# Kernel optimization log

Hardware: AMD Instinct MI355X
Metric: run time of the kernel (lower is better)

## Reference

```python
import jax, jax.numpy as jnp
import numpy as np

ROPE_DIM = 64
ROPE_THETA = 10000.0
SLIDING_WINDOW = 1024
_K_MASK = jnp.finfo(jnp.bfloat16).min


def _pos_embeddings(positions, head_dim, rope_theta):
    # positions: [B, T] -> sin, cos: [B, T, head_dim]
    fraction = jnp.arange(0, head_dim, 2, dtype=jnp.float32) / head_dim
    inv_freq = 1.0 / (rope_theta ** fraction)
    sinusoid = jnp.einsum('BT,k->BTk', positions.astype(jnp.float32), inv_freq,
                          precision=jax.lax.Precision.HIGHEST)
    sin = jnp.sin(sinusoid); cos = jnp.cos(sinusoid)
    return jnp.concatenate([sin, sin], -1), jnp.concatenate([cos, cos], -1)


def _rotate_half(x):
    x1, x2 = x[..., :x.shape[-1] // 2], x[..., x.shape[-1] // 2:]
    return jnp.concatenate([-x2, x1], -1)


def _apply_rope_partial(x, sin, cos, rope_dim):
    x_rope, x_nope = x[..., :rope_dim], x[..., rope_dim:]
    sin = sin[:, :, None, :]; cos = cos[:, :, None, :]
    x_rope = x_rope * cos + _rotate_half(x_rope) * sin
    return jnp.concatenate([x_rope, x_nope], -1).astype(x.dtype)


def setup_inputs() -> dict:
    key = jax.random.key(0)
    ks = jax.random.split(key, 6)
    B, T, D = 2, 2048, 2048
    N, K, H, Hv = 16, 4, 128, 128
    S = 2048  # cache size
    sc = 0.02
    return {
        'x': jax.random.normal(ks[0], (B, T, D), jnp.float32),
        'wq': jax.random.normal(ks[1], (D, N, H), jnp.float32) * sc,
        'wk': jax.random.normal(ks[2], (D, K, H), jnp.float32) * sc,
        'wv': jax.random.normal(ks[3], (D, K, Hv), jnp.float32) * sc,
        'wo': jax.random.normal(ks[4], (N, Hv, D), jnp.float32) * sc,
        'sink_bias': jnp.zeros((N,), jnp.float32),
        'k_cache': jnp.zeros((B, S, K, H), jnp.float32),
        'v_cache': jnp.zeros((B, S, K, Hv), jnp.float32),
        'segment_ids': jnp.ones((B, T), jnp.int32),
        'cur_ind': 0,
        'start_ind': -jnp.ones((B,), jnp.int32),
    }


def reference(x, wq, wk, wv, wo, sink_bias, k_cache, v_cache,
              segment_ids, cur_ind, start_ind):
    B, T, D = x.shape
    N, H = wq.shape[1], wq.shape[2]
    K, Hv = wk.shape[1], wv.shape[2]
    n_rep = N // K
    scaling = H ** -0.5
    cur_ind = jnp.asarray(cur_ind, jnp.int32)

    q = jnp.einsum('BTD,DNH->BTNH', x, wq)
    k = jnp.einsum('BSD,DKH->BSKH', x, wk)
    v = jnp.einsum('BSD,DKV->BSKV', x, wv)

    # left pads / positions from segment ids
    left_pads = jnp.sum(jnp.cumsum(segment_ids != 0, axis=-1) == 0, -1).astype(jnp.int32)
    start = jnp.where(start_ind < 0, left_pads, start_ind)
    pos = jax.vmap(lambda row: jnp.where(row != 0,
                                         jnp.arange(T, dtype=jnp.int32) - jnp.argmax(row).astype(jnp.int32),
                                         2 ** 30))(segment_ids) + cur_ind
    sin, cos = _pos_embeddings(pos, ROPE_DIM, ROPE_THETA)
    q = _apply_rope_partial(q, sin, cos, ROPE_DIM)
    k = _apply_rope_partial(k, sin, cos, ROPE_DIM)

    # KV cache append
    kc = jax.lax.dynamic_update_slice(k_cache, k, (0, cur_ind, 0, 0))
    vc = jax.lax.dynamic_update_slice(v_cache, v, (0, cur_ind, 0, 0))
    S = kc.shape[1]

    # GQA repeat
    kr = jnp.repeat(kc[:, :, :, None, :], n_rep, axis=3).reshape(B, S, N, H)
    vr = jnp.repeat(vc[:, :, :, None, :], n_rep, axis=3).reshape(B, S, N, Hv)

    logits = jnp.einsum('BTNH,BSNH->BTNS', q, kr) * scaling

    q_pos = cur_ind + jnp.arange(T, dtype=jnp.int32)[None, :] - start[:, None]
    ts = jnp.arange(S, dtype=jnp.int32)
    kv_seg = (ts[None, :] >= start[:, None]) & (ts[None, :] < cur_ind + T)
    k_pos = ts[None, :] - start[:, None]
    causal = k_pos[:, None, :] <= q_pos[:, :, None]
    seg_mask = kv_seg[:, None, :] == segment_ids[:, :, None]
    window = k_pos[:, None, :] >= q_pos[:, :, None] - (SLIDING_WINDOW - 1)
    final_mask = causal & seg_mask & window  # [B, T, S]
    logits = jnp.where(final_mask[:, :, None, :], logits, _K_MASK)

    # attention sink bias: extra softmax slot per head
    sink = jnp.broadcast_to(sink_bias[None, None, :, None], (B, T, N, 1))
    logits = jnp.concatenate([logits, sink], axis=-1)
    weights = jax.nn.softmax(logits.astype(jnp.float32), axis=-1).astype(logits.dtype)
    weights = weights[..., :-1]

    attn = jnp.einsum('BTNS,BSNV->BTNV', weights, vr)
    return jnp.einsum('BTNV,NVD->BTD', attn, wo)
```

## Files before the change

### kernel.cpp

```cpp
#include <hip/hip_runtime.h>
#include <hip/hip_bf16.h>
#include <stdint.h>

#define BB 2
#define TT 2048
#define DD 2048
#define NHQ 16
#define KH 4
#define HD 128
#define SS 2048
#define WINDOW 1024
#define M2FIX 12.0f
#define QSC_LOG2E 0.12751751f
#define LOG2E 1.4426950408889634f
#define NLOG2F 0.4152410118609203f

typedef __attribute__((ext_vector_type(8))) short bf16x8;
typedef __attribute__((ext_vector_type(4))) float f32x4;
typedef __attribute__((ext_vector_type(16))) float f32x16;

#define MFMA16(a, b, c) __builtin_amdgcn_mfma_f32_16x16x32_bf16(a, b, c, 0, 0, 0)
#define MFMA32(a, b, c) __builtin_amdgcn_mfma_f32_32x32x16_bf16(a, b, c, 0, 0, 0)

__device__ __forceinline__ ushort f2bf(float f) {
  uint32_t u = __float_as_uint(f);
  u += 0x7FFF + ((u >> 16) & 1);
  return (ushort)(u >> 16);
}
__device__ __forceinline__ ushort f2bf_trunc(float f) {
  return (ushort)(__float_as_uint(f) >> 16);
}
__device__ __forceinline__ float bf2f(ushort h) {
  return __uint_as_float(((uint32_t)h) << 16);
}

__device__ __forceinline__ void async_copy16(const ushort* g, ushort* l) {
  __builtin_amdgcn_global_load_lds(
      (const __attribute__((address_space(1))) uint32_t*)g,
      (__attribute__((address_space(3))) uint32_t*)l, 16, 0, 0);
}

__device__ __forceinline__ void tr_tile(const float* __restrict__ in,
                                        ushort* __restrict__ out,
                                        int C, int ldo, int cx, int cy) {
  __shared__ float tile[32][36];
  int t = threadIdx.x;
  int r0 = cy * 32, c0 = cx * 32;
  int row = t >> 3, c4 = (t & 7) * 4;
  float4 v = *(const float4*)&in[(size_t)(r0 + row) * C + c0 + c4];
  *(float4*)&tile[row][c4] = v;
  __syncthreads();
  int oc = t >> 3, or4 = (t & 7) * 4;
  ushort4 o;
  o.x = f2bf(tile[or4 + 0][oc]);
  o.y = f2bf(tile[or4 + 1][oc]);
  o.z = f2bf(tile[or4 + 2][oc]);
  o.w = f2bf(tile[or4 + 3][oc]);
  *(ushort4*)&out[(size_t)(c0 + oc) * ldo + r0 + or4] = o;
}

__global__ void prep_fused(const float* __restrict__ x, const float* __restrict__ wq,
                           const float* __restrict__ wk, const float* __restrict__ wv,
                           const float* __restrict__ wo, const int* __restrict__ seg,
                           const int* __restrict__ start_ind, ushort* __restrict__ xb,
                           ushort* __restrict__ WcatT, ushort* __restrict__ WoT,
                           int* __restrict__ meta) {
  int bz = blockIdx.x;
  int tid = threadIdx.x;
  if (bz < 2) {
    __shared__ int red[256];
    int b = bz;
    int first = TT;
    for (int t = tid; t < TT; t += 256)
      if (seg[b * TT + t] != 0) first = min(first, t);
    red[tid] = first;
    __syncthreads();
    for (int s = 128; s > 0; s >>= 1) {
      if (tid < s) red[tid] = min(red[tid], red[tid + s]);
      __syncthreads();
    }
    if (tid == 0) {
      int fi = red[0];
      int st = start_ind[b] < 0 ? fi : start_ind[b];
      meta[b * 2 + 0] = st;
      meta[b * 2 + 1] = (fi >= TT) ? 0 : fi;
    }
    return;
  }
  bz -= 2;
  if (bz < 2048) {
#pragma unroll
    for (int p = 0; p < 4; p++) {
      int i = bz * 1024 + p * 256 + tid;
      float4 v = ((const float4*)x)[i];
      ushort4 o;
      o.x = f2bf(v.x); o.y = f2bf(v.y); o.z = f2bf(v.z); o.w = f2bf(v.w);
      ((ushort4*)xb)[i] = o;
    }
    return;
  }
  bz -= 2048;
  if (bz < 4096) { tr_tile(wq, WcatT, 2048, 2048, bz & 63, bz >> 6); return; }
  bz -= 4096;
  if (bz < 1024) { tr_tile(wk, WcatT + (size_t)2048 * 2048, 512, 2048, bz & 15, bz >> 4); return; }
  bz -= 1024;
  if (bz < 1024) { tr_tile(wv, WcatT + (size_t)2560 * 2048, 512, 2048, bz & 15, bz >> 4); return; }
  bz -= 1024;
  tr_tile(wo, WoT, 2048, 2048, bz & 63, bz >> 6);
}

__global__ __launch_bounds__(256) void gemm_qkv(const ushort* __restrict__ A,
                                                const ushort* __restrict__ Bt,
                                                const int* __restrict__ seg,
                                                const int* __restrict__ cur_p,
                                                const int* __restrict__ meta,
                                                ushort* __restrict__ qa,
                                                ushort* __restrict__ ka,
                                                ushort* __restrict__ vat) {
  const int K = DD;
  __shared__ ushort SH[16640];
  ushort* As = SH;
  ushort* Bs = SH + 8192;
  float* posf_s = (float*)(SH + 16384);
  int tid = threadIdx.x;
  int lane = tid & 63, wave = tid >> 6;
  int wr = wave >> 1, wc = wave & 1;
  int orig = blockIdx.y * 24 + blockIdx.x;
  int wid = (orig & 7) * 96 + (orig >> 3);
  int by = wid / 24, bx = wid - by * 24;
  int row0 = by * 128, col0 = bx * 128;
  int l31 = lane & 31, khalf = lane >> 5, lx8 = l31 & 7;
  int cur = cur_p[0];

  if (tid < 128) {
    int m = row0 + tid;
    int bb = m >> 11, t = m & 2047;
    int segv = seg[m];
    int first = meta[bb * 2 + 1];
    posf_s[tid] = (segv != 0) ? (float)(t - first + cur) : 1073741824.0f;
  }

  f32x16 acc[2][2];
#pragma unroll
  for (int i = 0; i < 2; i++)
#pragma unroll
    for (int j = 0; j < 2; j++)
#pragma unroll
      for (int e = 0; e < 16; e++) acc[i][j][e] = 0.f;

  int srow = tid >> 3, scol = tid & 7;
  int ssw = (scol ^ (srow & 7)) * 8;
  const ushort* Ag = A  + (size_t)(row0 + srow) * K + ssw;
  const ushort* Bg = Bt + (size_t)(col0 + srow) * K + ssw;
  ushort* AsD = As + tid * 8;
  ushort* BsD = Bs + tid * 8;

  for (int kc = 0; kc < K; kc += 64) {
    __syncthreads();
#pragma unroll
    for (int p = 0; p < 4; p++)
      async_copy16(Ag + kc + (size_t)(p * 32) * K, AsD + p * 2048);
#pragma unroll
    for (int p = 0; p < 4; p++)
      async_copy16(Bg + kc + (size_t)(p * 32) * K, BsD + p * 2048);
    __syncthreads();
#pragma unroll
    for (int ks = 0; ks < 4; ks++) {
      bf16x8 af[2], bfm[2];
      int ch = (ks * 2 + khalf) ^ lx8;
#pragma unroll
      for (int i = 0; i < 2; i++)
        af[i] = *(const bf16x8*)(As + (wr * 64 + i * 32 + l31) * 64 + ch * 8);
#pragma unroll
      for (int j = 0; j < 2; j++)
        bfm[j] = *(const bf16x8*)(Bs + (wc * 64 + j * 32 + l31) * 64 + ch * 8);
#pragma unroll
      for (int i = 0; i < 2; i++)
#pragma unroll
        for (int j = 0; j < 2; j++)
          acc[i][j] = MFMA32(af[i], bfm[j], acc[i][j]);
    }
  }

  int cb0 = col0 + wc * 64;
  int region = (cb0 < 2048) ? 0 : (cb0 < 2560 ? 1 : 2);

  if (region <= 1) {
    bool ropehalf = ((cb0 & 64) == 0);
    int hbase = cb0 & 64;
    float invf = exp2f(-NLOG2F * (float)l31);
#pragma unroll
    for (int i = 0; i < 2; i++) {
#pragma unroll
      for (int reg = 0; reg < 16; reg++) {
        int rloc = wr * 64 + i * 32 + (reg & 3) + 8 * (reg >> 2) + 4 * khalf;
        int m = row0 + rloc;
        int b = m >> 11, t = m & 2047;
        float v0 = acc[i][0][reg], v1 = acc[i][1][reg];
        if (ropehalf) {
          float posf = posf_s[rloc];
          float sn, cs;
          __sincosf(posf * invf, &sn, &cs);
          float n0 = v0 * cs - v1 * sn;
          v1 = v1 * cs + v0 * sn;
          v0 = n0;
        }
        if (region == 0) {
          int head = cb0 >> 7;
          size_t base = ((size_t)(b * NHQ + head) * TT + t) * HD + hbase;
          qa[base + l31]      = f2bf(v0 * QSC_LOG2E);
          qa[base + 32 + l31] = f2bf(v1 * QSC_LOG2E);
        } else {
          int head = (cb0 - 2048) >> 7;
          size_t rowbase = ((size_t)(b * KH + head) * SS + t) * HD;
          int sw = t & 7;
          int c0x = hbase + l31, c1x = hbase + 32 + l31;
          ka[rowbase + ((((c0x >> 3) ^ sw) << 3) | (c0x & 7))] = f2bf(v0);
          ka[rowbase + ((((c1x >> 3) ^ sw) << 3) | (c1x & 7))] = f2bf(v1);
        }
      }
    }
  } else {
    __syncthreads();
    ushort* TB = SH;
    int hbase = wc * 64;
#pragma unroll
    for (int i = 0; i < 2; i++)
#pragma unroll
      for (int reg = 0; reg < 16; reg++) {
        int rloc = wr * 64 + i * 32 + (reg & 3) + 8 * (reg >> 2) + 4 * khalf;
        int h0 = hbase + l31, h1 = hbase + 32 + l31;
        TB[h0 * 128 + (rloc ^ ((h0 & 15) << 3))] = f2bf(acc[i][0][reg]);
        TB[h1 * 128 + (rloc ^ ((h1 & 15) << 3))] = f2bf(acc[i][1][reg]);
      }
    __syncthreads();
    int headv = (col0 - 2560) >> 7;
    int bv = row0 >> 11;
    ushort* vout = vat + (size_t)(bv * KH + headv) * HD * SS + (row0 & 2047);
#pragma unroll
    for (int pass = 0; pass < 8; pass++) {
      int idx = pass * 256 + tid;
      int h = idx >> 4, cc = idx & 15;
      int s64 = cc >> 3, c = cc & 7;
      bf16x8 vd = *(const bf16x8*)(TB + h * 128 + (s64 ^ ((h >> 3) & 1)) * 64 + c * 8);
      *(bf16x8*)(vout + (size_t)h * SS + s64 * 64 + c * 8) = vd;
    }
  }
}

template <int OUT_F32>
__global__ __launch_bounds__(256) void gemm_bt(const ushort* __restrict__ A,
                                               const ushort* __restrict__ Bt,
                                               void* __restrict__ Cout,
                                               int M, int N, int K) {
  __shared__ ushort As[128 * 64];
  __shared__ ushort Bs[128 * 64];
  int tid = threadIdx.x;
  int lane = tid & 63, wave = tid >> 6;
  int wr = wave >> 1, wc = wave & 1;
  int orig = blockIdx.y * gridDim.x + blockIdx.x;
  int nwg = gridDim.x * gridDim.y;
  int cpx = nwg >> 3;
  int wid = (orig & 7) * cpx + (orig >> 3);
  int by = wid / gridDim.x, bx = wid - by * gridDim.x;
  int row0 = by * 128, col0 = bx * 128;
  int l31 = lane & 31, khalf = lane >> 5, lx8 = l31 & 7;

  f32x16 acc[2][2];
#pragma unroll
  for (int i = 0; i < 2; i++)
#pragma unroll
    for (int j = 0; j < 2; j++)
#pragma unroll
      for (int e = 0; e < 16; e++) acc[i][j][e] = 0.f;

  int srow = tid >> 3, scol = tid & 7;
  int ssw = (scol ^ (srow & 7)) * 8;
  const ushort* Ag = A  + (size_t)(row0 + srow) * K + ssw;
  const ushort* Bg = Bt + (size_t)(col0 + srow) * K + ssw;
  ushort* AsD = As + tid * 8;
  ushort* BsD = Bs + tid * 8;

  for (int kc = 0; kc < K; kc += 64) {
    __syncthreads();
#pragma unroll
    for (int p = 0; p < 4; p++)
      async_copy16(Ag + kc + (size_t)(p * 32) * K, AsD + p * 2048);
#pragma unroll
    for (int p = 0; p < 4; p++)
      async_copy16(Bg + kc + (size_t)(p * 32) * K, BsD + p * 2048);
    __syncthreads();
#pragma unroll
    for (int ks = 0; ks < 4; ks++) {
      bf16x8 af[2], bfm[2];
      int ch = (ks * 2 + khalf) ^ lx8;
#pragma unroll
      for (int i = 0; i < 2; i++)
        af[i] = *(const bf16x8*)(As + (wr * 64 + i * 32 + l31) * 64 + ch * 8);
#pragma unroll
      for (int j = 0; j < 2; j++)
        bfm[j] = *(const bf16x8*)(Bs + (wc * 64 + j * 32 + l31) * 64 + ch * 8);
#pragma unroll
      for (int i = 0; i < 2; i++)
#pragma unroll
        for (int j = 0; j < 2; j++)
          acc[i][j] = MFMA32(af[i], bfm[j], acc[i][j]);
    }
  }

#pragma unroll
  for (int i = 0; i < 2; i++)
#pragma unroll
    for (int reg = 0; reg < 16; reg++) {
      int r = row0 + wr * 64 + i * 32 + (reg & 3) + 8 * (reg >> 2) + 4 * khalf;
#pragma unroll
      for (int j = 0; j < 2; j++) {
        int c = col0 + wc * 64 + j * 32 + l31;
        float v = acc[i][j][reg];
        if (OUT_F32)
          ((float*)Cout)[(size_t)r * N + c] = v;
        else
          ((ushort*)Cout)[(size_t)r * N + c] = f2bf(v);
      }
    }
}

__global__ __launch_bounds__(256) void flash_attn(
    const ushort* __restrict__ qa, const ushort* __restrict__ ka,
    const ushort* __restrict__ vat, const float* __restrict__ sink_bias,
    const int* __restrict__ seg, const int* __restrict__ cur_p,
    const int* __restrict__ meta, ushort* __restrict__ Obuf) {
  __shared__ ushort Ks[64 * 128];
  __shared__ ushort VT[128 * 64];
  __shared__ ushort Ps[4 * 16 * 64];

  int bx = blockIdx.x;
  int xcd = bx & 7;
  int b = xcd >> 2, kb = xcd & 3;
  int idx = bx >> 3;
  int g = idx & 31, s = idx >> 5;
  int n = kb * 4 + (g & 3);
  int j = g >> 2;
  int qt = (s == 0) ? j : (s == 1) ? (15 - j) : (s == 2) ? (16 + j) : (31 - j);
  int t0 = qt * 64;
  int cur = cur_p[0];
  int start = meta[b * 2];

  int tid = threadIdx.x, lane = tid & 63, w = tid >> 6;
  int lcol = lane & 15, quad = lane >> 4, lx = lcol & 7;
  int t0w = t0 + w * 16;

  const ushort* qbase = qa + (size_t)(b * NHQ + n) * TT * HD;
  const ushort* kbase = ka + (size_t)(b * KH + kb) * SS * HD;
  const ushort* vtb   = vat + (size_t)(b * KH + kb) * HD * SS;

  bf16x8 qf[4];
  {
    const ushort* qrow = qbase + (size_t)(t0w + lcol) * HD + quad * 8;
#pragma unroll
    for (int c = 0; c < 4; c++) qf[c] = *(const bf16x8*)(qrow + c * 32);
  }

  int segq[4], trow[4];
#pragma unroll
  for (int r = 0; r < 4; r++) {
    trow[r] = t0w + quad * 4 + r;
    segq[r] = seg[b * TT + trow[r]];
  }
  int seg1 = __all(segq[0] == 1 && segq[1] == 1 && segq[2] == 1 && segq[3] == 1);

  f32x4 oacc[8], lacc;
#pragma unroll
  for (int ob = 0; ob < 8; ob++) { f32x4 z = {0.f, 0.f, 0.f, 0.f}; oacc[ob] = z; }
  { f32x4 z = {0.f, 0.f, 0.f, 0.f}; lacc = z; }

  bf16x8 ones;
#pragma unroll
  for (int e = 0; e < 8; e++) ones[e] = (short)0x3F80;

  ushort* KsD = Ks + tid * 8;
  ushort* VTD = VT + tid * 8;
  const ushort* KgT = kbase + tid * 8;
  const ushort* VgT = vtb + (size_t)(tid >> 3) * SS + (tid & 7) * 8;

  int lo = cur + t0 - (WINDOW - 1); if (lo < 0) lo = 0;
  int hi = cur + t0 + 63;           if (hi > SS - 1) hi = SS - 1;
  int ktlo = lo >> 6, kthi = hi >> 6;

  ushort* PsW = Ps + w * 1024;

  for (int kt = ktlo; kt <= kthi; kt++) {
    int ks0 = kt * 64;
    __syncthreads();
#pragma unroll
    for (int p2 = 0; p2 < 4; p2++)
      async_copy16(KgT + (size_t)ks0 * 128 + p2 * 2048, KsD + p2 * 2048);
#pragma unroll
    for (int p2 = 0; p2 < 4; p2++)
      async_copy16(VgT + ks0 + (size_t)p2 * 32 * SS, VTD + p2 * 2048);
    __syncthreads();

    bool active = (ks0 <= cur + t0w + 15) && (ks0 + 63 >= cur + t0w - (WINDOW - 1));
    if (active) {
      f32x4 sacc[4];
#pragma unroll
      for (int cb = 0; cb < 4; cb++) { f32x4 z = {0.f, 0.f, 0.f, 0.f}; sacc[cb] = z; }
#pragma unroll
      for (int c = 0; c < 4; c++) {
#pragma unroll
        for (int cb = 0; cb < 4; cb++) {
          bf16x8 kf = *(const bf16x8*)(Ks + (cb * 16 + lcol) * 128 +
                                       (((c * 4 + quad) ^ lx)) * 8);
          sacc[cb] = MFMA16(qf[c], kf, sacc[cb]);
        }
      }

      bool fast = seg1 && (ks0 >= start) && (ks0 + 63 <= cur + t0w) &&
                  (ks0 >= cur + t0w + 15 - (WINDOW - 1));
      if (fast) {
#pragma unroll
        for (int r = 0; r < 4; r++) {
          int row = quad * 4 + r;
#pragma unroll
          for (int cb = 0; cb < 4; cb++) {
            float pv = exp2f(sacc[cb][r] - M2FIX);
            PsW[row * 64 + (((cb * 2 + (lcol >> 3)) ^ (row & 7)) * 8) + lx] = f2bf_trunc(pv);
          }
        }
      } else {
        int sidx[4], kvseg[4];
#pragma unroll
        for (int cb = 0; cb < 4; cb++) {
          sidx[cb] = ks0 + cb * 16 + lcol;
          kvseg[cb] = (sidx[cb] >= start && sidx[cb] < cur + TT) ? 1 : 0;
        }
#pragma unroll
        for (int r = 0; r < 4; r++) {
          int row = quad * 4 + r;
          int qp = (segq[r] != 0) ? (cur + trow[r]) : (1 << 29);
#pragma unroll
          for (int cb = 0; cb < 4; cb++) {
            bool ok = (sidx[cb] <= qp) && (sidx[cb] >= qp - (WINDOW - 1)) &&
                      (kvseg[cb] == segq[r]);
            float pv = ok ? exp2f(sacc[cb][r] - M2FIX) : 0.f;
            PsW[row * 64 + (((cb * 2 + (lcol >> 3)) ^ (row & 7)) * 8) + lx] = f2bf_trunc(pv);
          }
        }
      }

#pragma unroll
      for (int c2 = 0; c2 < 2; c2++) {
        bf16x8 pf = *(const bf16x8*)(PsW + lcol * 64 + (((c2 * 4 + quad) ^ lx)) * 8);
#pragma unroll
        for (int ob = 0; ob < 8; ob++) {
          bf16x8 vf = *(const bf16x8*)(VT + (ob * 16 + lcol) * 64 +
                                       (((c2 * 4 + quad) ^ lx)) * 8);
          oacc[ob] = MFMA16(pf, vf, oacc[ob]);
        }
        lacc = MFMA16(pf, ones, lacc);
      }
    }
  }

  float sb = sink_bias[n];
#pragma unroll
  for (int r = 0; r < 4; r++) {
    float l = lacc[r] + exp2f(sb * LOG2E - M2FIX);
    float inv = 1.f / l;
    int t = trow[r];
    size_t base = ((size_t)(b * TT + t)) * (NHQ * HD) + n * HD;
#pragma unroll
    for (int ob = 0; ob < 8; ob++)
      Obuf[base + ob * 16 + lcol] = f2bf(oacc[ob][r] * inv);
  }
}

extern "C" void kernel_launch(void* const* d_in, const int* in_sizes, int n_in,
                              void* d_out, int out_size, void* d_ws, size_t ws_size,
                              hipStream_t stream) {
  const float* x  = (const float*)d_in[0];
  const float* wq = (const float*)d_in[1];
  const float* wk = (const float*)d_in[2];
  const float* wv = (const float*)d_in[3];
  const float* wo = (const float*)d_in[4];
  const float* sink = (const float*)d_in[5];
  const int* seg = (const int*)d_in[8];
  const int* cur = (const int*)d_in[9];
  const int* start_ind = (const int*)d_in[10];

  char* ws = (char*)d_ws;
  ushort* xb    = (ushort*)(ws + 0);
  ushort* WcatT = (ushort*)(ws + 16777216);
  ushort* WoT   = (ushort*)(ws + 29360128);
  ushort* qa    = (ushort*)(ws + 37748736);
  ushort* ka    = (ushort*)(ws + 54525952);
  ushort* vat   = (ushort*)(ws + 62914560);
  ushort* Obuf  = (ushort*)(ws + 67108864);
  int*    meta  = (int*)(ws + 83886080);

  prep_fused<<<12290, 256, 0, stream>>>(x, wq, wk, wv, wo, seg, start_ind,
                                        xb, WcatT, WoT, meta);
  gemm_qkv<<<dim3(24, 32), 256, 0, stream>>>(xb, WcatT, seg, cur, meta, qa, ka, vat);
  flash_attn<<<1024, 256, 0, stream>>>(qa, ka, vat, sink, seg, cur, meta, Obuf);
  gemm_bt<1><<<dim3(16, 32), 256, 0, stream>>>(Obuf, WoT, d_out, 4096, 2048, 2048);
}
```

Before: 309.4 us.

## Double-buffer K/V tiles in flash attention to overlap loads with MFMA

```diff
diff --git a/kernel.cpp b/kernel.cpp
--- a/kernel.cpp
+++ b/kernel.cpp
@@ -330,8 +330,8 @@
     const ushort* __restrict__ vat, const float* __restrict__ sink_bias,
     const int* __restrict__ seg, const int* __restrict__ cur_p,
     const int* __restrict__ meta, ushort* __restrict__ Obuf) {
-  __shared__ ushort Ks[64 * 128];
-  __shared__ ushort VT[128 * 64];
+  __shared__ ushort Ks[2][64 * 128];
+  __shared__ ushort VT[2][128 * 64];
   __shared__ ushort Ps[4 * 16 * 64];
 
   int bx = blockIdx.x;
@@ -378,8 +378,6 @@
 #pragma unroll
   for (int e = 0; e < 8; e++) ones[e] = (short)0x3F80;
 
-  ushort* KsD = Ks + tid * 8;
-  ushort* VTD = VT + tid * 8;
   const ushort* KgT = kbase + tid * 8;
   const ushort* VgT = vtb + (size_t)(tid >> 3) * SS + (tid & 7) * 8;
 
@@ -389,19 +387,30 @@
 
   ushort* PsW = Ps + w * 1024;
 
+#define STAGE_KV(BUF, KS0)                                                    \
+  do {                                                                        \
+    _Pragma("unroll")                                                         \
+    for (int p2 = 0; p2 < 4; p2++)                                            \
+      async_copy16(KgT + (size_t)(KS0) * 128 + p2 * 2048,                     \
+                   &Ks[BUF][0] + tid * 8 + p2 * 2048);                        \
+    _Pragma("unroll")                                                         \
+    for (int p2 = 0; p2 < 4; p2++)                                            \
+      async_copy16(VgT + (KS0) + (size_t)p2 * 32 * SS,                        \
+                   &VT[BUF][0] + tid * 8 + p2 * 2048);                        \
+  } while (0)
+
+  STAGE_KV(0, ktlo * 64);
+  __syncthreads();
+
+  int buf = 0;
   for (int kt = ktlo; kt <= kthi; kt++) {
     int ks0 = kt * 64;
-    __syncthreads();
-#pragma unroll
-    for (int p2 = 0; p2 < 4; p2++)
-      async_copy16(KgT + (size_t)ks0 * 128 + p2 * 2048, KsD + p2 * 2048);
-#pragma unroll
-    for (int p2 = 0; p2 < 4; p2++)
-      async_copy16(VgT + ks0 + (size_t)p2 * 32 * SS, VTD + p2 * 2048);
-    __syncthreads();
+    if (kt < kthi) STAGE_KV(buf ^ 1, ks0 + 64);
 
     bool active = (ks0 <= cur + t0w + 15) && (ks0 + 63 >= cur + t0w - (WINDOW - 1));
     if (active) {
+      const ushort* KsB = &Ks[buf][0];
+      const ushort* VTB = &VT[buf][0];
       f32x4 sacc[4];
 #pragma unroll
       for (int cb = 0; cb < 4; cb++) { f32x4 z = {0.f, 0.f, 0.f, 0.f}; sacc[cb] = z; }
@@ -409,7 +418,7 @@
       for (int c = 0; c < 4; c++) {
 #pragma unroll
         for (int cb = 0; cb < 4; cb++) {
-          bf16x8 kf = *(const bf16x8*)(Ks + (cb * 16 + lcol) * 128 +
+          bf16x8 kf = *(const bf16x8*)(KsB + (cb * 16 + lcol) * 128 +
                                        (((c * 4 + quad) ^ lx)) * 8);
           sacc[cb] = MFMA16(qf[c], kf, sacc[cb]);
         }
@@ -453,14 +462,18 @@
         bf16x8 pf = *(const bf16x8*)(PsW + lcol * 64 + (((c2 * 4 + quad) ^ lx)) * 8);
 #pragma unroll
         for (int ob = 0; ob < 8; ob++) {
-          bf16x8 vf = *(const bf16x8*)(VT + (ob * 16 + lcol) * 64 +
+          bf16x8 vf = *(const bf16x8*)(VTB + (ob * 16 + lcol) * 64 +
                                        (((c2 * 4 + quad) ^ lx)) * 8);
           oacc[ob] = MFMA16(pf, vf, oacc[ob]);
         }
         lacc = MFMA16(pf, ones, lacc);
       }
     }
-  }
+
+    __syncthreads();
+    buf ^= 1;
+  }
+#undef STAGE_KV
 
   float sb = sink_bias[n];
 #pragma unroll
```

Result: no change. 311.4 us (+0.7%).
